# Performance work log

Hardware: AMD Instinct MI355X
Metric: run time of the kernel (lower is better)

Reference implementation:

```python
import jax, jax.numpy as jnp
import numpy as np

BATCH = 8192
VOCAB = 16384
EMBED = 256
EPS = 1e-6


def setup_inputs() -> dict:
    key = jax.random.key(0)
    k1, k2 = jax.random.split(key)
    # multi-hot indicator input: values in {0,1}; only nonzero positions matter
    x = jax.random.randint(k1, (BATCH, VOCAB), 0, 2, dtype=jnp.int32)
    # learned embedding table (nn.Embedding weight)
    emb = jax.random.normal(k2, (VOCAB, EMBED), dtype=jnp.float32)
    return {"x": x, "emb": emb}


def reference(x, emb):
    # torch: gather embeddings at nonzero (row, col) pairs, scatter-add per row,
    # divide by per-row nonzero count (+eps). Equivalent jit-friendly form:
    # mask @ emb gives the per-row sum of embeddings over nonzero columns.
    mask = (x != 0).astype(emb.dtype)               # [B, V]
    embed_sum = mask @ emb                           # [B, E]
    count = jnp.sum(mask, axis=1, keepdims=True) + EPS  # [B, 1]
    return embed_sum / count
```

## Files before the change

kernel.cpp:

```cpp
#include <hip/hip_runtime.h>
#include <hip/hip_bf16.h>
#include <stdint.h>

#define BATCH 8192
#define VOCAB 16384
#define EMBED 256

#define BM 64
#define BK 64
#define KSPLIT 8
#define KRANGE (VOCAB / KSPLIT)
#define KITERS (KRANGE / BK)
#define MTILES (BATCH / BM)

typedef __attribute__((ext_vector_type(4))) float    f32x4;
typedef __attribute__((ext_vector_type(4))) int      i32x4;
typedef __attribute__((ext_vector_type(4))) unsigned u32x4;

#define EMB_WS_BYTES ((size_t)VOCAB * EMBED * 2)
#define CNT_WS_BYTES ((size_t)KSPLIT * BATCH * 4)
#define PART_STRIDE  ((size_t)BATCH * EMBED)

__device__ __forceinline__ void gload_lds16(const void* g, void* l) {
    __builtin_amdgcn_global_load_lds(
        (const __attribute__((address_space(1))) unsigned int*)(uintptr_t)g,
        (__attribute__((address_space(3))) unsigned int*)(uint32_t)(uintptr_t)l,
        16, 0, 0);
}

__device__ __forceinline__ void mfma_bf16(f32x4& acc, i32x4 a, i32x4 b) {
    asm("v_mfma_f32_16x16x32_bf16 %0, %1, %2, %0" : "+v"(acc) : "v"(a), "v"(b));
}

__global__ __launch_bounds__(256) void prep_kernel(
    const float* __restrict__ emb, unsigned short* __restrict__ emb_ws)
{
    int t = blockIdx.x * 256 + threadIdx.x;
    int ko = t >> 8;
    int e  = t & 255;
    union { unsigned short s[8]; u32x4 q; } v;
    #pragma unroll
    for (int j = 0; j < 8; ++j) {
        float f = emb[(size_t)(ko * 8 + j) * EMBED + e];
        unsigned u = __float_as_uint(f);
        u += 0x7FFFu + ((u >> 16) & 1u);
        v.s[j] = (unsigned short)(u >> 16);
    }
    int kt  = ko >> 3;
    int kk0 = (ko & 7) * 8;
    unsigned byt = (unsigned)(e * 128 + ((kk0 * 2) ^ ((e & 7) << 4)));
    *(u32x4*)((char*)emb_ws + (size_t)kt * 32768 + byt) = v.q;
}

__global__ __launch_bounds__(256, 4) void gemm_kernel(
    const int* __restrict__ x, const unsigned short* __restrict__ emb_ws,
    float* __restrict__ part_ws, int* __restrict__ cnt_ws)
{
    __shared__ __align__(16) unsigned short As[BM * BK];
    __shared__ __align__(16) unsigned short Bs[EMBED * BK];

    int bid   = blockIdx.x;
    int split = bid & (KSPLIT - 1);
    int mt    = bid >> 3;

    int tid  = threadIdx.x;
    int lane = tid & 63;
    int wave = tid >> 6;

    int ar = tid >> 2;
    int aq = tid & 3;
    const int*  aptr  = x + (size_t)(mt * BM + ar) * VOCAB + split * KRANGE + aq * 4;
    const char* bbase = (const char*)emb_ws + (size_t)split * KITERS * 32768;

    int cnt = 0;
    f32x4 acc[4][4];
    #pragma unroll
    for (int i = 0; i < 4; ++i)
        #pragma unroll
        for (int j = 0; j < 4; ++j) acc[i][j] = (f32x4){0.f, 0.f, 0.f, 0.f};

    for (int kt = 0; kt < KITERS; ++kt) {
        const char* bsrc = bbase + (size_t)kt * 32768 + tid * 16;
        #pragma unroll
        for (int i = 0; i < 8; ++i)
            gload_lds16(bsrc + i * 4096, (char*)Bs + tid * 16 + i * 4096);

        const int* ap = aptr + kt * BK;
        i32x4 av[4];
        #pragma unroll
        for (int j = 0; j < 4; ++j) av[j] = *(const i32x4*)(ap + j * 16);

        #pragma unroll
        for (int j = 0; j < 4; ++j) {
            unsigned lo = (av[j].x ? 0x3F80u : 0u) | (av[j].y ? 0x3F800000u : 0u);
            unsigned hi = (av[j].z ? 0x3F80u : 0u) | (av[j].w ? 0x3F800000u : 0u);
            cnt += (av[j].x != 0) + (av[j].y != 0) + (av[j].z != 0) + (av[j].w != 0);
            int kk = aq * 4 + j * 16;
            unsigned byt = (unsigned)(ar * 128 + ((kk * 2) ^ ((ar & 7) << 4)));
            *(uint2*)((char*)As + byt) = make_uint2(lo, hi);
        }

        __syncthreads();

        #pragma unroll
        for (int ks = 0; ks < 2; ++ks) {
            int kg = ks * 32 + (lane >> 4) * 8;
            i32x4 af[4], bf[4];
            #pragma unroll
            for (int fm = 0; fm < 4; ++fm) {
                int row = fm * 16 + (lane & 15);
                af[fm] = *(const i32x4*)((const char*)As + row * 128 +
                                         ((kg * 2) ^ ((row & 7) << 4)));
            }
            #pragma unroll
            for (int fe = 0; fe < 4; ++fe) {
                int e = wave * 64 + fe * 16 + (lane & 15);
                bf[fe] = *(const i32x4*)((const char*)Bs + e * 128 +
                                         ((kg * 2) ^ ((e & 7) << 4)));
            }
            #pragma unroll
            for (int fm = 0; fm < 4; ++fm)
                #pragma unroll
                for (int fe = 0; fe < 4; ++fe)
                    mfma_bf16(acc[fm][fe], af[fm], bf[fe]);
        }
        __syncthreads();
    }

    cnt += __shfl_xor(cnt, 1);
    cnt += __shfl_xor(cnt, 2);
    if (aq == 0) cnt_ws[split * BATCH + mt * BM + ar] = cnt;

    #pragma unroll
    for (int fm = 0; fm < 4; ++fm)
        #pragma unroll
        for (int fe = 0; fe < 4; ++fe)
            asm volatile("s_nop 7\n\ts_nop 7" : "+v"(acc[fm][fe]));

    float* part = part_ws + (size_t)split * PART_STRIDE;
    #pragma unroll
    for (int fm = 0; fm < 4; ++fm) {
        int row = mt * BM + fm * 16 + (lane >> 4) * 4;
        #pragma unroll
        for (int fe = 0; fe < 4; ++fe) {
            int col = wave * 64 + fe * 16 + (lane & 15);
            float* p = part + (size_t)row * EMBED + col;
            #pragma unroll
            for (int r = 0; r < 4; ++r)
                p[(size_t)r * EMBED] = acc[fm][fe][r];
        }
    }
}

__global__ __launch_bounds__(256) void div_kernel(
    float* __restrict__ out, const float* __restrict__ part_ws,
    const int* __restrict__ cnt_ws)
{
    int t = blockIdx.x * 256 + threadIdx.x;
    int b = t >> 6;
    int c = 0;
    #pragma unroll
    for (int s = 0; s < KSPLIT; ++s) c += cnt_ws[s * BATCH + b];
    float inv = 1.0f / ((float)c + 1e-6f);
    f32x4 v = (f32x4){0.f, 0.f, 0.f, 0.f};
    #pragma unroll
    for (int s = 0; s < KSPLIT; ++s) {
        f32x4 p = ((const f32x4*)(part_ws + s * PART_STRIDE))[t];
        v.x += p.x; v.y += p.y; v.z += p.z; v.w += p.w;
    }
    v.x *= inv; v.y *= inv; v.z *= inv; v.w *= inv;
    ((f32x4*)out)[t] = v;
}

extern "C" void kernel_launch(void* const* d_in, const int* in_sizes, int n_in,
                              void* d_out, int out_size, void* d_ws, size_t ws_size,
                              hipStream_t stream)
{
    const int*   x   = (const int*)d_in[0];
    const float* emb = (const float*)d_in[1];
    float*       out = (float*)d_out;

    unsigned short* emb_ws  = (unsigned short*)d_ws;
    int*            cnt_ws  = (int*)((char*)d_ws + EMB_WS_BYTES);
    float*          part_ws = (float*)((char*)d_ws + EMB_WS_BYTES + CNT_WS_BYTES);

    prep_kernel<<<2048, 256, 0, stream>>>(emb, emb_ws);
    gemm_kernel<<<MTILES * KSPLIT, 256, 0, stream>>>(x, emb_ws, part_ws, cnt_ws);
    div_kernel<<<2048, 256, 0, stream>>>(out, part_ws, cnt_ws);
}
```

Baseline: 747.4 us.

## Double-buffer LDS tiles and software-pipeline the split-K GEMM loop

The GEMM main loop now uses two LDS buffers for both the mask tile and the embedding tile. The next B tile is loaded asynchronously and the next-next A tile is prefetched into registers while MFMAs run on the current tile. The two full __syncthreads per iteration are replaced with one barrier plus an explicit partial vmcnt wait, with scheduling barriers to keep the order fixed. LDS use per block doubles, so the occupancy hint drops from 4 to 2 blocks per CU, trading latency hiding through occupancy for latency hiding through overlap.

```diff
diff --git a/kernel.cpp b/kernel.cpp
--- a/kernel.cpp
+++ b/kernel.cpp
@@ -52,12 +52,71 @@
     *(u32x4*)((char*)emb_ws + (size_t)kt * 32768 + byt) = v.q;
 }
 
-__global__ __launch_bounds__(256, 4) void gemm_kernel(
+__device__ __forceinline__ void stage_B(const char* bbase, int kt, char* bs, int tid) {
+    const char* src = bbase + (size_t)kt * 32768 + tid * 16;
+    #pragma unroll
+    for (int i = 0; i < 8; ++i)
+        gload_lds16(src + i * 4096, bs + tid * 16 + i * 4096);
+}
+
+__device__ __forceinline__ void load_A(const int* aptr, int kt, i32x4 (&av)[4]) {
+    const int* ap = aptr + kt * BK;
+    #pragma unroll
+    for (int j = 0; j < 4; ++j) av[j] = *(const i32x4*)(ap + j * 16);
+}
+
+__device__ __forceinline__ void pack_A(const i32x4 (&av)[4], char* as_buf,
+                                       int ar, int aq, int& cnt, bool docnt) {
+    #pragma unroll
+    for (int j = 0; j < 4; ++j) {
+        unsigned lo = (av[j].x ? 0x3F80u : 0u) | (av[j].y ? 0x3F800000u : 0u);
+        unsigned hi = (av[j].z ? 0x3F80u : 0u) | (av[j].w ? 0x3F800000u : 0u);
+        if (docnt)
+            cnt += (av[j].x != 0) + (av[j].y != 0) + (av[j].z != 0) + (av[j].w != 0);
+        int kk = aq * 4 + j * 16;
+        unsigned byt = (unsigned)(ar * 128 + ((kk * 2) ^ ((ar & 7) << 4)));
+        *(uint2*)(as_buf + byt) = make_uint2(lo, hi);
+    }
+}
+
+__device__ __forceinline__ void compute_tile(const char* as_buf, const char* bs_buf,
+                                             int lane, int wave, f32x4 (&acc)[4][4]) {
+    #pragma unroll
+    for (int ks = 0; ks < 2; ++ks) {
+        int kg = ks * 32 + (lane >> 4) * 8;
+        i32x4 af[4], bf[4];
+        #pragma unroll
+        for (int fm = 0; fm < 4; ++fm) {
+            int row = fm * 16 + (lane & 15);
+            af[fm] = *(const i32x4*)(as_buf + row * 128 + ((kg * 2) ^ ((row & 7) << 4)));
+        }
+        #pragma unroll
+        for (int fe = 0; fe < 4; ++fe) {
+            int e = wave * 64 + fe * 16 + (lane & 15);
+            bf[fe] = *(const i32x4*)(bs_buf + e * 128 + ((kg * 2) ^ ((e & 7) << 4)));
+        }
+        #pragma unroll
+        for (int fm = 0; fm < 4; ++fm)
+            #pragma unroll
+            for (int fe = 0; fe < 4; ++fe)
+                mfma_bf16(acc[fm][fe], af[fm], bf[fe]);
+    }
+}
+
+#define PIPE_BARRIER() do {                                   \
+    __builtin_amdgcn_sched_barrier(0);                        \
+    asm volatile("s_waitcnt vmcnt(4) lgkmcnt(0)" ::: "memory"); \
+    __builtin_amdgcn_sched_barrier(0);                        \
+    __builtin_amdgcn_s_barrier();                             \
+    __builtin_amdgcn_sched_barrier(0);                        \
+} while (0)
+
+__global__ __launch_bounds__(256, 2) void gemm_kernel(
     const int* __restrict__ x, const unsigned short* __restrict__ emb_ws,
     float* __restrict__ part_ws, int* __restrict__ cnt_ws)
 {
-    __shared__ __align__(16) unsigned short As[BM * BK];
-    __shared__ __align__(16) unsigned short Bs[EMBED * BK];
+    __shared__ __align__(16) unsigned short As[2][BM * BK];
+    __shared__ __align__(16) unsigned short Bs[2][EMBED * BK];
 
     int bid   = blockIdx.x;
     int split = bid & (KSPLIT - 1);
@@ -79,52 +138,27 @@
         #pragma unroll
         for (int j = 0; j < 4; ++j) acc[i][j] = (f32x4){0.f, 0.f, 0.f, 0.f};
 
-    for (int kt = 0; kt < KITERS; ++kt) {
-        const char* bsrc = bbase + (size_t)kt * 32768 + tid * 16;
-        #pragma unroll
-        for (int i = 0; i < 8; ++i)
-            gload_lds16(bsrc + i * 4096, (char*)Bs + tid * 16 + i * 4096);
-
-        const int* ap = aptr + kt * BK;
-        i32x4 av[4];
-        #pragma unroll
-        for (int j = 0; j < 4; ++j) av[j] = *(const i32x4*)(ap + j * 16);
-
-        #pragma unroll
-        for (int j = 0; j < 4; ++j) {
-            unsigned lo = (av[j].x ? 0x3F80u : 0u) | (av[j].y ? 0x3F800000u : 0u);
-            unsigned hi = (av[j].z ? 0x3F80u : 0u) | (av[j].w ? 0x3F800000u : 0u);
-            cnt += (av[j].x != 0) + (av[j].y != 0) + (av[j].z != 0) + (av[j].w != 0);
-            int kk = aq * 4 + j * 16;
-            unsigned byt = (unsigned)(ar * 128 + ((kk * 2) ^ ((ar & 7) << 4)));
-            *(uint2*)((char*)As + byt) = make_uint2(lo, hi);
-        }
-
-        __syncthreads();
-
-        #pragma unroll
-        for (int ks = 0; ks < 2; ++ks) {
-            int kg = ks * 32 + (lane >> 4) * 8;
-            i32x4 af[4], bf[4];
-            #pragma unroll
-            for (int fm = 0; fm < 4; ++fm) {
-                int row = fm * 16 + (lane & 15);
-                af[fm] = *(const i32x4*)((const char*)As + row * 128 +
-                                         ((kg * 2) ^ ((row & 7) << 4)));
-            }
-            #pragma unroll
-            for (int fe = 0; fe < 4; ++fe) {
-                int e = wave * 64 + fe * 16 + (lane & 15);
-                bf[fe] = *(const i32x4*)((const char*)Bs + e * 128 +
-                                         ((kg * 2) ^ ((e & 7) << 4)));
-            }
-            #pragma unroll
-            for (int fm = 0; fm < 4; ++fm)
-                #pragma unroll
-                for (int fe = 0; fe < 4; ++fe)
-                    mfma_bf16(acc[fm][fe], af[fm], bf[fe]);
-        }
-        __syncthreads();
+    i32x4 av[4];
+
+    load_A(aptr, 0, av);
+    stage_B(bbase, 0, (char*)Bs[0], tid);
+    pack_A(av, (char*)As[0], ar, aq, cnt, true);
+    __builtin_amdgcn_sched_barrier(0);
+    load_A(aptr, 1, av);
+    PIPE_BARRIER();
+
+    int cur = 0;
+    for (int t = 0; t < KITERS; ++t) {
+        int tB = (t + 1 < KITERS) ? t + 1 : KITERS - 1;
+        stage_B(bbase, tB, (char*)Bs[cur ^ 1], tid);
+        __builtin_amdgcn_sched_barrier(0);
+        compute_tile((const char*)As[cur], (const char*)Bs[cur], lane, wave, acc);
+        pack_A(av, (char*)As[cur ^ 1], ar, aq, cnt, t + 1 < KITERS);
+        __builtin_amdgcn_sched_barrier(0);
+        int tA = (t + 2 < KITERS) ? t + 2 : 0;
+        load_A(aptr, tA, av);
+        PIPE_BARRIER();
+        cur ^= 1;
     }
 
     cnt += __shfl_xor(cnt, 1);
```

New measurement: 748.1 us. No clear change (+0.1%).
